# Optimization experiments

Measured on AMD Instinct MI355X. Metric: run time of the kernel, lower is better.

## Reference

```python
import jax, jax.numpy as jnp
import numpy as np

B, S, D = 2, 2048, 1024
H, DH = 16, 64  # num_heads, qk/vo embed size per head
NEG_INF = -1e9


def setup_inputs() -> dict:
    key = jax.random.key(0)
    ks = jax.random.split(key, 7)
    return {
        "query": jax.random.normal(ks[0], (B, S, D), jnp.float32),
        "key": jax.random.normal(ks[1], (B, S, D), jnp.float32),
        "value": jax.random.normal(ks[2], (B, S, D), jnp.float32),
        "Wq": jax.random.normal(ks[3], (D, D), jnp.float32) * 0.02,
        "Wk": jax.random.normal(ks[4], (D, D), jnp.float32) * 0.02,
        "Wv": jax.random.normal(ks[5], (D, D), jnp.float32) * 0.02,
        "Wo": jax.random.normal(ks[6], (D, D), jnp.float32) * 0.02,
    }


def reference(query, key, value, Wq, Wk, Wv, Wo):
    # projections (nn.Linear, no bias): y = x @ W.T
    q = (query @ Wq.T).reshape(B, S, H, DH)
    k = (key @ Wk.T).reshape(B, S, H, DH)
    v = (value @ Wv.T).reshape(B, S, H, DH)
    # scores normalized by sqrt(per-head qk embed dim)
    scores = jnp.einsum("bqhd,bkhd->bhqk", q, k) / jnp.sqrt(jnp.float32(DH))
    # causal mask
    causal = jnp.tril(jnp.ones((S, S), dtype=bool))
    scores = jnp.where(causal[None, None, :, :], scores, NEG_INF)
    attn = jax.nn.softmax(scores, axis=-1)  # attention_type='softmax'
    ctx = jnp.einsum("bhqk,bkhd->bqhd", attn, v).reshape(B, S, H * DH)
    return ctx @ Wo.T
```

## Files before the change

### kernel.cpp

```cpp
#include <hip/hip_runtime.h>
#include <hip/hip_bf16.h>
#include <cstdint>


typedef __attribute__((ext_vector_type(8))) __bf16 bf16x8;
typedef __attribute__((ext_vector_type(8))) unsigned short ushort8;
typedef __attribute__((ext_vector_type(4))) float f32x4;
typedef unsigned short ushort_t;

#define B_ 2
#define S_ 2048
#define D_ 1024
#define H_ 16
#define DH_ 64
#define BK 64

#define QSCALE 0.1803368801111244f

__device__ __forceinline__ ushort_t f2b(float f) {
  uint32_t u = __builtin_bit_cast(uint32_t, f);
  u += 0x7fffu + ((u >> 16) & 1u);
  return (ushort_t)(u >> 16);
}

__device__ __forceinline__ f32x4 mfma16(bf16x8 a, bf16x8 b, f32x4 c) {
  return __builtin_amdgcn_mfma_f32_16x16x32_bf16(a, b, c, 0, 0, 0);
}

__device__ __forceinline__ void gload16(const ushort_t* g, char* lds) {
  __builtin_amdgcn_global_load_lds(
      (__attribute__((address_space(1))) void*)(uintptr_t)g,
      (__attribute__((address_space(3))) void*)(uintptr_t)lds, 16, 0, 0);
}

__global__ __launch_bounds__(256) void cvt3_kernel(
    const float* __restrict__ s0, const float* __restrict__ s1,
    const float* __restrict__ s2, ushort_t* __restrict__ d0,
    ushort_t* __restrict__ d1, ushort_t* __restrict__ d2) {
  const float* src = blockIdx.y == 0 ? s0 : (blockIdx.y == 1 ? s1 : s2);
  ushort_t* dst = blockIdx.y == 0 ? d0 : (blockIdx.y == 1 ? d1 : d2);
  int i = blockIdx.x * 256 + threadIdx.x;
  f32x4 a = ((const f32x4*)src)[i * 2];
  f32x4 b = ((const f32x4*)src)[i * 2 + 1];
  ushort8 o;
#pragma unroll
  for (int j = 0; j < 4; ++j) o[j] = f2b(a[j]);
#pragma unroll
  for (int j = 0; j < 4; ++j) o[4 + j] = f2b(b[j]);
  ((ushort8*)dst)[i] = o;
}

__global__ __launch_bounds__(256) void cvt4_kernel(
    const float* __restrict__ s0, const float* __restrict__ s1,
    const float* __restrict__ s2, const float* __restrict__ s3,
    ushort_t* __restrict__ d0, ushort_t* __restrict__ d1,
    ushort_t* __restrict__ d2, ushort_t* __restrict__ d3) {
  const float* src = blockIdx.y == 0 ? s0
                     : (blockIdx.y == 1 ? s1 : (blockIdx.y == 2 ? s2 : s3));
  ushort_t* dst = blockIdx.y == 0 ? d0
                  : (blockIdx.y == 1 ? d1 : (blockIdx.y == 2 ? d2 : d3));
  int i = blockIdx.x * 256 + threadIdx.x;
  f32x4 a = ((const f32x4*)src)[i * 2];
  f32x4 b = ((const f32x4*)src)[i * 2 + 1];
  ushort8 o;
#pragma unroll
  for (int j = 0; j < 4; ++j) o[j] = f2b(a[j]);
#pragma unroll
  for (int j = 0; j < 4; ++j) o[4 + j] = f2b(b[j]);
  ((ushort8*)dst)[i] = o;
}

template <int TBM, int TBN, int OUTF32>
__device__ __forceinline__ void gemm_body(const ushort_t* __restrict__ A,
                                          const ushort_t* __restrict__ W,
                                          void* __restrict__ Cout,
                                          int M, int N, int K, float scale,
                                          int i0, int j0) {
  constexpr int MI = TBM / 32, NJ = TBN / 32;
  __shared__ char smem[(TBM + TBN) * BK * 2];
  char* sA = smem;
  char* sB = smem + TBM * BK * 2;
  const int tid = threadIdx.x;
  const int w = tid >> 6, lane = tid & 63, l16 = lane & 15, lg = lane >> 4;
  const int wr = (w >> 1) * (TBM / 2), wc = (w & 1) * (TBN / 2);
  f32x4 acc[MI][NJ] = {};
  const int nk = K / BK;
  for (int kt = 0; kt < nk; ++kt) {
    const int k0 = kt * BK;
    __syncthreads();
#pragma unroll
    for (int is = 0; is < MI; ++is) {
      int chunk = is * 256 + tid;
      int row = chunk >> 3, s = chunk & 7, sl = s ^ (row & 7);
      gload16(A + (size_t)(i0 + row) * K + k0 + sl * 8, sA + (is * 4 + w) * 1024);
    }
#pragma unroll
    for (int is = 0; is < NJ; ++is) {
      int chunk = is * 256 + tid;
      int row = chunk >> 3, s = chunk & 7, sl = s ^ (row & 7);
      gload16(W + (size_t)(j0 + row) * K + k0 + sl * 8, sB + (is * 4 + w) * 1024);
    }
    __syncthreads();
#pragma unroll
    for (int ks = 0; ks < 2; ++ks) {
      bf16x8 af[MI], bfr[NJ];
#pragma unroll
      for (int mi = 0; mi < MI; ++mi) {
        int r = wr + mi * 16 + l16;
        af[mi] = *(const bf16x8*)(sA + r * 128 + ((ks * 64 + lg * 16) ^ ((r & 7) << 4)));
      }
#pragma unroll
      for (int nj = 0; nj < NJ; ++nj) {
        int r = wc + nj * 16 + l16;
        bfr[nj] = *(const bf16x8*)(sB + r * 128 + ((ks * 64 + lg * 16) ^ ((r & 7) << 4)));
      }
#pragma unroll
      for (int mi = 0; mi < MI; ++mi)
#pragma unroll
        for (int nj = 0; nj < NJ; ++nj)
          acc[mi][nj] = mfma16(af[mi], bfr[nj], acc[mi][nj]);
    }
  }
#pragma unroll
  for (int mi = 0; mi < MI; ++mi)
#pragma unroll
    for (int nj = 0; nj < NJ; ++nj)
#pragma unroll
      for (int r = 0; r < 4; ++r) {
        int row = i0 + wr + mi * 16 + lg * 4 + r;
        int col = j0 + wc + nj * 16 + l16;
        float v = acc[mi][nj][r] * scale;
        if (OUTF32)
          ((float*)Cout)[(size_t)row * N + col] = v;
        else
          ((ushort_t*)Cout)[(size_t)row * N + col] = f2b(v);
      }
}

__global__ __launch_bounds__(256) void qkv_gemm(
    const ushort_t* __restrict__ xq, const ushort_t* __restrict__ xk,
    const ushort_t* __restrict__ xv, const ushort_t* __restrict__ wq,
    const ushort_t* __restrict__ wk, const ushort_t* __restrict__ wv,
    ushort_t* __restrict__ Qb, ushort_t* __restrict__ Kb,
    ushort_t* __restrict__ Vt) {
  const int z = blockIdx.z;
  if (z < 2) {
    gemm_body<128, 128, 0>(z ? xk : xq, z ? wk : wq, z ? Kb : Qb,
                           B_ * S_, D_, D_, z ? 1.f : QSCALE,
                           blockIdx.x * 128, blockIdx.y * 128);
  } else {
    gemm_body<128, 128, 0>(wv, xv, Vt, D_, B_ * S_, D_, 1.f,
                           blockIdx.y * 128, blockIdx.x * 128);
  }
}

__global__ __launch_bounds__(256) void out_gemm(const ushort_t* __restrict__ ctx,
                                                const ushort_t* __restrict__ wo,
                                                float* __restrict__ out) {
  gemm_body<128, 64, 1>(ctx, wo, out, B_ * S_, D_, D_, 1.f,
                        blockIdx.y * 128, blockIdx.x * 64);
}

__global__ __launch_bounds__(256) void attn_kernel(
    const ushort_t* __restrict__ Qb, const ushort_t* __restrict__ Kb,
    const ushort_t* __restrict__ VtG, ushort_t* __restrict__ ctx) {
  const int pair = blockIdx.x;
  const int bh = blockIdx.y;
  const int b = bh >> 4, h = bh & 15;
  const int tid = threadIdx.x;
  const int w = tid >> 6, lane = tid & 63, l16 = lane & 15, lg = lane >> 4;

  __shared__ char smem[2 * 16384 + 4 * 2048];
  char* sP = smem + 32768 + w * 2048;

  const size_t BS = (size_t)B_ * S_;
  const size_t qkbase = ((size_t)b * S_) * D_ + h * DH_;
  const ushort_t* Vbase = VtG + (size_t)(h * 64) * BS + (size_t)b * S_;

  for (int sub = 0; sub < 2; ++sub) {
    const int qt = sub ? (31 - pair) : pair;
    const int q0 = qt * 64 + w * 16;
    const int tl = qt;

    bf16x8 qf[2];
    {
      const ushort_t* qrow = Qb + qkbase + (size_t)(q0 + l16) * D_;
      qf[0] = *(const bf16x8*)(qrow + lg * 8);
      qf[1] = *(const bf16x8*)(qrow + 32 + lg * 8);
    }

    f32x4 acc_o[4] = {};
    float m[4], lsum[4];
#pragma unroll
    for (int r = 0; r < 4; ++r) { m[r] = -1e30f; lsum[r] = 0.f; }

    int cur = 0;
    {
      const ushort_t* Ksrc = Kb + qkbase;
      const ushort_t* Vsrc = Vbase;
#pragma unroll
      for (int it = 0; it < 2; ++it) {
        int chunk = it * 256 + tid;
        int row = chunk >> 3, s = chunk & 7, sl = s ^ (row & 7);
        gload16(Ksrc + (size_t)row * D_ + sl * 8, smem + (it * 4 + w) * 1024);
        gload16(Vsrc + (size_t)row * BS + sl * 8, smem + 8192 + (it * 4 + w) * 1024);
      }
    }
    __syncthreads();

    for (int t = 0; t <= tl; ++t) {
      if (t < tl) {
        char* bK = smem + (cur ^ 1) * 16384;
        const ushort_t* Ksrc = Kb + qkbase + (size_t)((t + 1) * 64) * D_;
        const ushort_t* Vsrc = Vbase + (t + 1) * 64;
#pragma unroll
        for (int it = 0; it < 2; ++it) {
          int chunk = it * 256 + tid;
          int row = chunk >> 3, s = chunk & 7, sl = s ^ (row & 7);
          gload16(Ksrc + (size_t)row * D_ + sl * 8, bK + (it * 4 + w) * 1024);
          gload16(Vsrc + (size_t)row * BS + sl * 8, bK + 8192 + (it * 4 + w) * 1024);
        }
      }
      char* bK = smem + cur * 16384;
      char* bV = bK + 8192;

      f32x4 sc[4] = {};
#pragma unroll
      for (int ks = 0; ks < 2; ++ks)
#pragma unroll
        for (int nt = 0; nt < 4; ++nt) {
          int rk = nt * 16 + l16;
          bf16x8 kf = *(const bf16x8*)(bK + rk * 128 + ((ks * 64 + lg * 16) ^ ((rk & 7) << 4)));
          sc[nt] = mfma16(qf[ks], kf, sc[nt]);
        }
      if (t == tl) {
#pragma unroll
        for (int nt = 0; nt < 4; ++nt)
#pragma unroll
          for (int r = 0; r < 4; ++r) {
            int kg = t * 64 + nt * 16 + l16;
            int qg = q0 + lg * 4 + r;
            if (kg > qg) sc[nt][r] = -1e30f;
          }
      }
      float alpha[4];
#pragma unroll
      for (int r = 0; r < 4; ++r) {
        float v = fmaxf(fmaxf(sc[0][r], sc[1][r]), fmaxf(sc[2][r], sc[3][r]));
        v = fmaxf(v, __shfl_xor(v, 1));
        v = fmaxf(v, __shfl_xor(v, 2));
        v = fmaxf(v, __shfl_xor(v, 4));
        v = fmaxf(v, __shfl_xor(v, 8));
        float mn = fmaxf(m[r], v);
        alpha[r] = exp2f(m[r] - mn);
        m[r] = mn;
      }
      float rsum[4] = {0.f, 0.f, 0.f, 0.f};
#pragma unroll
      for (int nt = 0; nt < 4; ++nt)
#pragma unroll
        for (int r = 0; r < 4; ++r) {
          float p = exp2f(sc[nt][r] - m[r]);
          rsum[r] += p;
          int prow = lg * 4 + r;
          int kv = nt * 16 + l16;
          *(ushort_t*)(sP + prow * 128 + ((kv * 2) ^ ((prow & 7) << 4))) = f2b(p);
        }
#pragma unroll
      for (int r = 0; r < 4; ++r) {
        float v = rsum[r];
        v += __shfl_xor(v, 1);
        v += __shfl_xor(v, 2);
        v += __shfl_xor(v, 4);
        v += __shfl_xor(v, 8);
        lsum[r] = lsum[r] * alpha[r] + v;
      }
#pragma unroll
      for (int nt = 0; nt < 4; ++nt)
#pragma unroll
        for (int r = 0; r < 4; ++r) acc_o[nt][r] *= alpha[r];
#pragma unroll
      for (int ks = 0; ks < 2; ++ks) {
        bf16x8 pa = *(const bf16x8*)(sP + l16 * 128 + ((ks * 64 + lg * 16) ^ ((l16 & 7) << 4)));
#pragma unroll
        for (int nt = 0; nt < 4; ++nt) {
          int dr = nt * 16 + l16;
          bf16x8 vb = *(const bf16x8*)(bV + dr * 128 + ((ks * 64 + lg * 16) ^ ((dr & 7) << 4)));
          acc_o[nt] = mfma16(pa, vb, acc_o[nt]);
        }
      }
      __syncthreads();
      cur ^= 1;
    }
#pragma unroll
    for (int r = 0; r < 4; ++r) {
      float inv = 1.f / lsum[r];
      int qg = q0 + lg * 4 + r;
      ushort_t* crow = ctx + qkbase + (size_t)qg * D_;
#pragma unroll
      for (int nt = 0; nt < 4; ++nt) crow[nt * 16 + l16] = f2b(acc_o[nt][r] * inv);
    }
  }
}

extern "C" void kernel_launch(void* const* d_in, const int* in_sizes, int n_in,
                              void* d_out, int out_size, void* d_ws, size_t ws_size,
                              hipStream_t stream) {
  const float* query = (const float*)d_in[0];
  const float* key   = (const float*)d_in[1];
  const float* value = (const float*)d_in[2];
  const float* Wq    = (const float*)d_in[3];
  const float* Wk    = (const float*)d_in[4];
  const float* Wv    = (const float*)d_in[5];
  const float* Wo    = (const float*)d_in[6];

  char* ws = (char*)d_ws;
  const size_t SZ = (size_t)B_ * S_ * D_ * 2;
  const size_t WSZ = (size_t)D_ * D_ * 2;
  ushort_t* xq  = (ushort_t*)(ws + 0 * SZ);
  ushort_t* xk  = (ushort_t*)(ws + 1 * SZ);
  ushort_t* xv  = (ushort_t*)(ws + 2 * SZ);
  ushort_t* Qb  = (ushort_t*)(ws + 3 * SZ);
  ushort_t* Kb  = (ushort_t*)(ws + 4 * SZ);
  ushort_t* Vt  = (ushort_t*)(ws + 5 * SZ);
  ushort_t* ctx = xq;
  ushort_t* wqb = (ushort_t*)(ws + 6 * SZ + 0 * WSZ);
  ushort_t* wkb = (ushort_t*)(ws + 6 * SZ + 1 * WSZ);
  ushort_t* wvb = (ushort_t*)(ws + 6 * SZ + 2 * WSZ);
  ushort_t* wob = (ushort_t*)(ws + 6 * SZ + 3 * WSZ);

  const int n8a = B_ * S_ * D_ / 8;
  const int n8w = D_ * D_ / 8;
  cvt3_kernel<<<dim3(n8a / 256, 3), 256, 0, stream>>>(query, key, value, xq, xk, xv);
  cvt4_kernel<<<dim3(n8w / 256, 4), 256, 0, stream>>>(Wq, Wk, Wv, Wo, wqb, wkb, wvb, wob);

  qkv_gemm<<<dim3(32, 8, 3), 256, 0, stream>>>(xq, xk, xv, wqb, wkb, wvb, Qb, Kb, Vt);

  attn_kernel<<<dim3(16, B_ * H_), 256, 0, stream>>>(Qb, Kb, Vt, ctx);

  out_gemm<<<dim3(D_ / 64, (B_ * S_) / 128), 256, 0, stream>>>(ctx, wob, (float*)d_out);
}
```

Measured before the change: 241.2 us.

## Transpose score MFMA, lazily rescale softmax, double-buffer out GEMM

The attention kernel now computes S^T by swapping MFMA operands, so each lane owns one query row. Row max and sum then need only two cross-lane shuffles, and the running max is rescaled only when some row's max actually grows. P is written to LDS as packed 4-element vectors with a cheaper round-to-nearest bf16 conversion, and s_setprio wraps the MFMA sections. The grid is reordered so blocks of the same q-tile pair run together, and the output GEMM switches to a new double-buffered gemm_db. These changes add shuffles to broadcast alpha and lsum back to the accumulator layout, and the bf16 conversion rounding changes slightly.

```diff
diff --git a/kernel.cpp b/kernel.cpp
--- a/kernel.cpp
+++ b/kernel.cpp
@@ -5,6 +5,7 @@
 
 typedef __attribute__((ext_vector_type(8))) __bf16 bf16x8;
 typedef __attribute__((ext_vector_type(8))) unsigned short ushort8;
+typedef __attribute__((ext_vector_type(4))) unsigned short usv4;
 typedef __attribute__((ext_vector_type(4))) float f32x4;
 typedef unsigned short ushort_t;
 
@@ -21,6 +22,10 @@
   uint32_t u = __builtin_bit_cast(uint32_t, f);
   u += 0x7fffu + ((u >> 16) & 1u);
   return (ushort_t)(u >> 16);
+}
+__device__ __forceinline__ ushort_t f2bf(float f) {
+  uint32_t u = __builtin_bit_cast(uint32_t, f);
+  return (ushort_t)((u + 0x8000u) >> 16);
 }
 
 __device__ __forceinline__ f32x4 mfma16(bf16x8 a, bf16x8 b, f32x4 c) {
@@ -137,6 +142,84 @@
       }
 }
 
+template <int TBM, int TBN, int OUTF32>
+__device__ __forceinline__ void gemm_db(const ushort_t* __restrict__ A,
+                                        const ushort_t* __restrict__ W,
+                                        void* __restrict__ Cout,
+                                        int M, int N, int K, float scale,
+                                        int i0, int j0) {
+  constexpr int MI = TBM / 32, NJ = TBN / 32;
+  constexpr int BUFB = (TBM + TBN) * BK * 2;
+  __shared__ char smem[2 * BUFB];
+  const int tid = threadIdx.x;
+  const int w = tid >> 6, lane = tid & 63, l16 = lane & 15, lg = lane >> 4;
+  const int wr = (w >> 1) * (TBM / 2), wc = (w & 1) * (TBN / 2);
+  f32x4 acc[MI][NJ] = {};
+  const int nk = K / BK;
+
+  auto stage = [&](int kt, int buf) {
+    char* sA = smem + buf * BUFB;
+    char* sB = sA + TBM * BK * 2;
+    const int k0 = kt * BK;
+#pragma unroll
+    for (int is = 0; is < MI; ++is) {
+      int chunk = is * 256 + tid;
+      int row = chunk >> 3, s = chunk & 7, sl = s ^ (row & 7);
+      gload16(A + (size_t)(i0 + row) * K + k0 + sl * 8, sA + (is * 4 + w) * 1024);
+    }
+#pragma unroll
+    for (int is = 0; is < NJ; ++is) {
+      int chunk = is * 256 + tid;
+      int row = chunk >> 3, s = chunk & 7, sl = s ^ (row & 7);
+      gload16(W + (size_t)(j0 + row) * K + k0 + sl * 8, sB + (is * 4 + w) * 1024);
+    }
+  };
+
+  stage(0, 0);
+  __syncthreads();
+  int cur = 0;
+  for (int kt = 0; kt < nk; ++kt) {
+    if (kt + 1 < nk) stage(kt + 1, cur ^ 1);
+    char* sA = smem + cur * BUFB;
+    char* sB = sA + TBM * BK * 2;
+#pragma unroll
+    for (int ks = 0; ks < 2; ++ks) {
+      bf16x8 af[MI], bfr[NJ];
+#pragma unroll
+      for (int mi = 0; mi < MI; ++mi) {
+        int r = wr + mi * 16 + l16;
+        af[mi] = *(const bf16x8*)(sA + r * 128 + ((ks * 64 + lg * 16) ^ ((r & 7) << 4)));
+      }
+#pragma unroll
+      for (int nj = 0; nj < NJ; ++nj) {
+        int r = wc + nj * 16 + l16;
+        bfr[nj] = *(const bf16x8*)(sB + r * 128 + ((ks * 64 + lg * 16) ^ ((r & 7) << 4)));
+      }
+#pragma unroll
+      for (int mi = 0; mi < MI; ++mi)
+#pragma unroll
+        for (int nj = 0; nj < NJ; ++nj)
+          acc[mi][nj] = mfma16(af[mi], bfr[nj], acc[mi][nj]);
+    }
+    __syncthreads();
+    cur ^= 1;
+  }
+#pragma unroll
+  for (int mi = 0; mi < MI; ++mi)
+#pragma unroll
+    for (int nj = 0; nj < NJ; ++nj)
+#pragma unroll
+      for (int r = 0; r < 4; ++r) {
+        int row = i0 + wr + mi * 16 + lg * 4 + r;
+        int col = j0 + wc + nj * 16 + l16;
+        float v = acc[mi][nj][r] * scale;
+        if (OUTF32)
+          ((float*)Cout)[(size_t)row * N + col] = v;
+        else
+          ((ushort_t*)Cout)[(size_t)row * N + col] = f2b(v);
+      }
+}
+
 __global__ __launch_bounds__(256) void qkv_gemm(
     const ushort_t* __restrict__ xq, const ushort_t* __restrict__ xk,
     const ushort_t* __restrict__ xv, const ushort_t* __restrict__ wq,
@@ -157,15 +240,15 @@
 __global__ __launch_bounds__(256) void out_gemm(const ushort_t* __restrict__ ctx,
                                                 const ushort_t* __restrict__ wo,
                                                 float* __restrict__ out) {
-  gemm_body<128, 64, 1>(ctx, wo, out, B_ * S_, D_, D_, 1.f,
-                        blockIdx.y * 128, blockIdx.x * 64);
+  gemm_db<128, 64, 1>(ctx, wo, out, B_ * S_, D_, D_, 1.f,
+                      blockIdx.y * 128, blockIdx.x * 64);
 }
 
 __global__ __launch_bounds__(256) void attn_kernel(
     const ushort_t* __restrict__ Qb, const ushort_t* __restrict__ Kb,
     const ushort_t* __restrict__ VtG, ushort_t* __restrict__ ctx) {
-  const int pair = blockIdx.x;
-  const int bh = blockIdx.y;
+  const int bh = blockIdx.x;
+  const int pair = blockIdx.y;
   const int b = bh >> 4, h = bh & 15;
   const int tid = threadIdx.x;
   const int w = tid >> 6, lane = tid & 63, l16 = lane & 15, lg = lane >> 4;
@@ -177,34 +260,39 @@
   const size_t qkbase = ((size_t)b * S_) * D_ + h * DH_;
   const ushort_t* Vbase = VtG + (size_t)(h * 64) * BS + (size_t)b * S_;
 
+  const int srow = tid >> 3, sslot = (tid & 7) ^ (srow & 7);
+  const size_t koff0 = (size_t)srow * D_ + sslot * 8;
+  const size_t koff1 = koff0 + (size_t)32 * D_;
+  const size_t voff0 = (size_t)srow * BS + sslot * 8;
+  const size_t voff1 = voff0 + (size_t)32 * BS;
+  const int dst0 = w * 1024, dst1 = 4096 + w * 1024;
+
+  const int pwsw = (l16 & 7) << 4;
+  const int pbase = l16 * 128;
+
   for (int sub = 0; sub < 2; ++sub) {
     const int qt = sub ? (31 - pair) : pair;
     const int q0 = qt * 64 + w * 16;
+    const int qg0 = q0 + l16;
     const int tl = qt;
 
     bf16x8 qf[2];
     {
-      const ushort_t* qrow = Qb + qkbase + (size_t)(q0 + l16) * D_;
+      const ushort_t* qrow = Qb + qkbase + (size_t)qg0 * D_;
       qf[0] = *(const bf16x8*)(qrow + lg * 8);
       qf[1] = *(const bf16x8*)(qrow + 32 + lg * 8);
     }
 
     f32x4 acc_o[4] = {};
-    float m[4], lsum[4];
-#pragma unroll
-    for (int r = 0; r < 4; ++r) { m[r] = -1e30f; lsum[r] = 0.f; }
+    float m = -1e30f, lsum = 0.f;
 
     int cur = 0;
     {
       const ushort_t* Ksrc = Kb + qkbase;
-      const ushort_t* Vsrc = Vbase;
-#pragma unroll
-      for (int it = 0; it < 2; ++it) {
-        int chunk = it * 256 + tid;
-        int row = chunk >> 3, s = chunk & 7, sl = s ^ (row & 7);
-        gload16(Ksrc + (size_t)row * D_ + sl * 8, smem + (it * 4 + w) * 1024);
-        gload16(Vsrc + (size_t)row * BS + sl * 8, smem + 8192 + (it * 4 + w) * 1024);
-      }
+      gload16(Ksrc + koff0, smem + dst0);
+      gload16(Ksrc + koff1, smem + dst1);
+      gload16(Vbase + voff0, smem + 8192 + dst0);
+      gload16(Vbase + voff1, smem + 8192 + dst1);
     }
     __syncthreads();
 
@@ -213,75 +301,72 @@
         char* bK = smem + (cur ^ 1) * 16384;
         const ushort_t* Ksrc = Kb + qkbase + (size_t)((t + 1) * 64) * D_;
         const ushort_t* Vsrc = Vbase + (t + 1) * 64;
-#pragma unroll
-        for (int it = 0; it < 2; ++it) {
-          int chunk = it * 256 + tid;
-          int row = chunk >> 3, s = chunk & 7, sl = s ^ (row & 7);
-          gload16(Ksrc + (size_t)row * D_ + sl * 8, bK + (it * 4 + w) * 1024);
-          gload16(Vsrc + (size_t)row * BS + sl * 8, bK + 8192 + (it * 4 + w) * 1024);
-        }
+        gload16(Ksrc + koff0, bK + dst0);
+        gload16(Ksrc + koff1, bK + dst1);
+        gload16(Vsrc + voff0, bK + 8192 + dst0);
+        gload16(Vsrc + voff1, bK + 8192 + dst1);
       }
       char* bK = smem + cur * 16384;
       char* bV = bK + 8192;
 
       f32x4 sc[4] = {};
+      __builtin_amdgcn_s_setprio(1);
 #pragma unroll
       for (int ks = 0; ks < 2; ++ks)
 #pragma unroll
         for (int nt = 0; nt < 4; ++nt) {
           int rk = nt * 16 + l16;
           bf16x8 kf = *(const bf16x8*)(bK + rk * 128 + ((ks * 64 + lg * 16) ^ ((rk & 7) << 4)));
-          sc[nt] = mfma16(qf[ks], kf, sc[nt]);
+          sc[nt] = mfma16(kf, qf[ks], sc[nt]);
         }
+      __builtin_amdgcn_s_setprio(0);
       if (t == tl) {
 #pragma unroll
         for (int nt = 0; nt < 4; ++nt)
 #pragma unroll
           for (int r = 0; r < 4; ++r) {
-            int kg = t * 64 + nt * 16 + l16;
-            int qg = q0 + lg * 4 + r;
-            if (kg > qg) sc[nt][r] = -1e30f;
+            int kg = t * 64 + nt * 16 + lg * 4 + r;
+            if (kg > qg0) sc[nt][r] = -1e30f;
           }
       }
-      float alpha[4];
-#pragma unroll
-      for (int r = 0; r < 4; ++r) {
-        float v = fmaxf(fmaxf(sc[0][r], sc[1][r]), fmaxf(sc[2][r], sc[3][r]));
-        v = fmaxf(v, __shfl_xor(v, 1));
-        v = fmaxf(v, __shfl_xor(v, 2));
-        v = fmaxf(v, __shfl_xor(v, 4));
-        v = fmaxf(v, __shfl_xor(v, 8));
-        float mn = fmaxf(m[r], v);
-        alpha[r] = exp2f(m[r] - mn);
-        m[r] = mn;
-      }
-      float rsum[4] = {0.f, 0.f, 0.f, 0.f};
+      float v = sc[0][0];
 #pragma unroll
       for (int nt = 0; nt < 4; ++nt)
 #pragma unroll
+        for (int r = 0; r < 4; ++r) v = fmaxf(v, sc[nt][r]);
+      v = fmaxf(v, __shfl_xor(v, 16));
+      v = fmaxf(v, __shfl_xor(v, 32));
+      if (!__all(v <= m)) {
+        float mn = fmaxf(m, v);
+        float alpha = exp2f(m - mn);
+        m = mn;
+        lsum *= alpha;
+#pragma unroll
         for (int r = 0; r < 4; ++r) {
-          float p = exp2f(sc[nt][r] - m[r]);
-          rsum[r] += p;
-          int prow = lg * 4 + r;
-          int kv = nt * 16 + l16;
-          *(ushort_t*)(sP + prow * 128 + ((kv * 2) ^ ((prow & 7) << 4))) = f2b(p);
+          float ar = __shfl(alpha, lg * 4 + r);
+#pragma unroll
+          for (int nt = 0; nt < 4; ++nt) acc_o[nt][r] *= ar;
         }
-#pragma unroll
-      for (int r = 0; r < 4; ++r) {
-        float v = rsum[r];
-        v += __shfl_xor(v, 1);
-        v += __shfl_xor(v, 2);
-        v += __shfl_xor(v, 4);
-        v += __shfl_xor(v, 8);
-        lsum[r] = lsum[r] * alpha[r] + v;
-      }
-#pragma unroll
-      for (int nt = 0; nt < 4; ++nt)
-#pragma unroll
-        for (int r = 0; r < 4; ++r) acc_o[nt][r] *= alpha[r];
+      }
+      float rs = 0.f;
+#pragma unroll
+      for (int nt = 0; nt < 4; ++nt) {
+        usv4 pk;
+#pragma unroll
+        for (int r = 0; r < 4; ++r) {
+          float p = exp2f(sc[nt][r] - m);
+          rs += p;
+          pk[r] = f2bf(p);
+        }
+        *(usv4*)(sP + pbase + ((nt * 32 + lg * 8) ^ pwsw)) = pk;
+      }
+      rs += __shfl_xor(rs, 16);
+      rs += __shfl_xor(rs, 32);
+      lsum += rs;
+      __builtin_amdgcn_s_setprio(1);
 #pragma unroll
       for (int ks = 0; ks < 2; ++ks) {
-        bf16x8 pa = *(const bf16x8*)(sP + l16 * 128 + ((ks * 64 + lg * 16) ^ ((l16 & 7) << 4)));
+        bf16x8 pa = *(const bf16x8*)(sP + pbase + ((ks * 64 + lg * 16) ^ pwsw));
 #pragma unroll
         for (int nt = 0; nt < 4; ++nt) {
           int dr = nt * 16 + l16;
@@ -289,12 +374,13 @@
           acc_o[nt] = mfma16(pa, vb, acc_o[nt]);
         }
       }
+      __builtin_amdgcn_s_setprio(0);
       __syncthreads();
       cur ^= 1;
     }
 #pragma unroll
     for (int r = 0; r < 4; ++r) {
-      float inv = 1.f / lsum[r];
+      float inv = 1.f / __shfl(lsum, lg * 4 + r);
       int qg = q0 + lg * 4 + r;
       ushort_t* crow = ctx + qkbase + (size_t)qg * D_;
 #pragma unroll
@@ -336,7 +422,7 @@
 
   qkv_gemm<<<dim3(32, 8, 3), 256, 0, stream>>>(xq, xk, xv, wqb, wkb, wvb, Qb, Kb, Vt);
 
-  attn_kernel<<<dim3(16, B_ * H_), 256, 0, stream>>>(Qb, Kb, Vt, ctx);
+  attn_kernel<<<dim3(B_ * H_, 16), 256, 0, stream>>>(Qb, Kb, Vt, ctx);
 
   out_gemm<<<dim3(D_ / 64, (B_ * S_) / 128), 256, 0, stream>>>(ctx, wob, (float*)d_out);
 }
```

New measurement: 217.5 us. 9.8% less time.
